# Optimization experiments

Hardware: AMD Instinct MI355X
Metric: run time of the kernel (lower is better)

Reference implementation:

```python
import jax, jax.numpy as jnp
import numpy as np
import math

L, B, E, H = 1024, 16, 512, 8
NUM_REL = 2 * L - 1  # 2047


def setup_inputs() -> dict:
    key = jax.random.key(0)
    ks = jax.random.split(key, 9)
    s = 0.02
    query = jax.random.normal(ks[0], (L, B, E), dtype=jnp.float32)
    return {
        "query": query,
        "key": jax.random.normal(ks[1], (L, B, E), dtype=jnp.float32),
        "value": jax.random.normal(ks[2], (L, B, E), dtype=jnp.float32),
        "in_proj_weight": jax.random.normal(ks[3], (3 * E, E), dtype=jnp.float32) * s,
        "in_proj_bias": jax.random.normal(ks[4], (3 * E,), dtype=jnp.float32) * s,
        "out_proj_weight": jax.random.normal(ks[5], (E, E), dtype=jnp.float32) * s,
        "out_proj_bias": jax.random.normal(ks[6], (E,), dtype=jnp.float32) * s,
        "rpe_weight_table": jax.random.normal(ks[7], (H, NUM_REL), dtype=jnp.float32) * s,
        "rpe_indices": jax.random.randint(ks[8], (L, L), 0, NUM_REL, dtype=jnp.int32),
    }


def _heads(x, w, b):
    # x: (N, Bn, E), w: (E, E), b: (E,) -> (Bn, H, N, d)
    n, bn, e = x.shape
    d = e // H
    y = jnp.einsum('nbe,fe->nbf', x, w) + b
    return y.reshape(n, bn, H, d).transpose(1, 2, 0, 3)


def reference(query, key, value, in_proj_weight, in_proj_bias, out_proj_weight,
              out_proj_bias, rpe_weight_table, rpe_indices):
    l, bn, e = query.shape
    d = e // H
    wq, wk, wv = jnp.split(in_proj_weight, 3, axis=0)
    bq, bk, bv = jnp.split(in_proj_bias, 3, axis=0)
    q = _heads(query, wq, bq)   # (B, H, L, d)
    k = _heads(key, wk, bk)     # (B, H, S, d)
    v = _heads(value, wv, bv)   # (B, H, S, d)
    q = q / math.sqrt(d)
    # rel-pos bias: gather table -> (H, L, S), broadcast over batch
    bias = rpe_weight_table[:, rpe_indices]
    attn = jnp.einsum('bhld,bhsd->bhls', q, k) + bias[None]
    attn = jax.nn.softmax(attn, axis=-1)
    out = jnp.einsum('bhls,bhsd->bhld', attn, v)   # (B, H, L, d)
    out = out.transpose(2, 0, 1, 3).reshape(l, bn, e)  # (L, B, E)
    out = jnp.einsum('lbe,fe->lbf', out, out_proj_weight) + out_proj_bias
    return out
```

## Files before the change

kernel.cpp:

```cpp
#include <hip/hip_runtime.h>
#include <hip/hip_bf16.h>


#define L_SEQ 1024
#define B_N   16
#define E_DIM 512
#define H_N   8
#define NREL  2047

typedef _Float16 f16;
using half8   = __attribute__((ext_vector_type(8))) _Float16;
using floatx4 = __attribute__((ext_vector_type(4))) float;

__device__ __forceinline__ half8 cvt8(const float4 a, const float4 b) {
    half8 h;
    h[0] = (f16)a.x; h[1] = (f16)a.y; h[2] = (f16)a.z; h[3] = (f16)a.w;
    h[4] = (f16)b.x; h[5] = (f16)b.y; h[6] = (f16)b.z; h[7] = (f16)b.w;
    return h;
}

__device__ __forceinline__ void gl_lds16(const void* g, void* l) {
    __builtin_amdgcn_global_load_lds(
        (const __attribute__((address_space(1))) unsigned int*)g,
        (__attribute__((address_space(3))) unsigned int*)l,
        16, 0, 0);
}

__global__ __launch_bounds__(256) void qkv_kernel(
    const float* __restrict__ Xq, const float* __restrict__ Xk, const float* __restrict__ Xv,
    const float* __restrict__ W, const float* __restrict__ Bias,
    f16* __restrict__ Qo, f16* __restrict__ Ko, f16* __restrict__ Vo)
{
    const int flat = blockIdx.x;
    const int xcd  = flat & 7;
    const int slot = flat >> 3;
    const int g    = xcd * 48 + (slot >> 2);
    const int f0   = (slot & 3) << 7;
    const int proj = g >> 7;
    const int n0   = (g & 127) << 7;

    const float* X  = (proj == 0) ? Xq : (proj == 1) ? Xk : Xv;
    const float* Wp = W + (size_t)(proj << 9) * E_DIM;

    __shared__ __align__(16) float As[128 * 32];
    __shared__ __align__(16) float Bs[128 * 32];

    const int tid  = threadIdx.x;
    const int w    = tid >> 6;
    const int lane = tid & 63;
    const int quad = lane >> 4, c = lane & 15;
    const int wm = (w >> 1) << 6, wn = (w & 1) << 6;

    const int lr = lane >> 3;
    const int lc = (lane & 7) ^ lr;
    const float* Xg = X  + (size_t)(n0 + (w << 3) + lr) * E_DIM + (lc << 2);
    const float* Wg = Wp + (size_t)(f0 + (w << 3) + lr) * E_DIM + (lc << 2);

    const int sa0 = (((quad << 1) ^ (c & 7)) << 2);
    const int sa1 = sa0 ^ 4;

    floatx4 acc[4][4] = {};

    for (int k0 = 0; k0 < E_DIM; k0 += 32) {
        __syncthreads();
#pragma unroll
        for (int i = 0; i < 4; ++i) {
            gl_lds16(Xg + (size_t)i * (32 * E_DIM) + k0, &As[((i << 5) + (w << 3)) << 5]);
            gl_lds16(Wg + (size_t)i * (32 * E_DIM) + k0, &Bs[((i << 5) + (w << 3)) << 5]);
        }
        __syncthreads();

        half8 a[4], bfr[4];
#pragma unroll
        for (int mt = 0; mt < 4; ++mt) {
            const int r = (wm + mt * 16 + c) << 5;
            const float4 lo = *reinterpret_cast<const float4*>(&As[r + sa0]);
            const float4 hi = *reinterpret_cast<const float4*>(&As[r + sa1]);
            a[mt] = cvt8(lo, hi);
        }
#pragma unroll
        for (int nt = 0; nt < 4; ++nt) {
            const int r = (wn + nt * 16 + c) << 5;
            const float4 lo = *reinterpret_cast<const float4*>(&Bs[r + sa0]);
            const float4 hi = *reinterpret_cast<const float4*>(&Bs[r + sa1]);
            bfr[nt] = cvt8(lo, hi);
        }
#pragma unroll
        for (int mt = 0; mt < 4; ++mt)
#pragma unroll
            for (int nt = 0; nt < 4; ++nt)
                acc[mt][nt] = __builtin_amdgcn_mfma_f32_16x16x32_f16(a[mt], bfr[nt], acc[mt][nt], 0, 0, 0);
    }

    f16* Dst = (proj == 0) ? Qo : (proj == 1) ? Ko : Vo;
    const float scale = (proj == 0) ? 0.125f : 1.0f;

#pragma unroll
    for (int nt = 0; nt < 4; ++nt) {
        const int fl = f0 + wn + nt * 16 + c;
        const float bj = Bias[(proj << 9) + fl];
        const int h = fl >> 6, d = fl & 63;
#pragma unroll
        for (int mt = 0; mt < 4; ++mt) {
#pragma unroll
            for (int r = 0; r < 4; ++r) {
                const int n = n0 + wm + mt * 16 + quad * 4 + r;
                const int l = n >> 4, b = n & 15;
                Dst[((((size_t)b * H_N + h) * L_SEQ + l) << 6) + d] =
                    (f16)((acc[mt][nt][r] + bj) * scale);
            }
        }
    }
}

__global__ __launch_bounds__(256) void transpose_v(
    const f16* __restrict__ V, f16* __restrict__ Vt)
{
    const int l0 = blockIdx.x << 6;
    const size_t base = (size_t)blockIdx.y << 16;
    __shared__ __align__(16) f16 T[64][72];
    const int tid = threadIdx.x;
    const int r = tid >> 2, co = (tid & 3) << 4;

    const uint4 a0 = *reinterpret_cast<const uint4*>(V + base + (size_t)(l0 + r) * 64 + co);
    const uint4 a1 = *reinterpret_cast<const uint4*>(V + base + (size_t)(l0 + r) * 64 + co + 8);
    *reinterpret_cast<uint4*>(&T[r][co])     = a0;
    *reinterpret_cast<uint4*>(&T[r][co + 8]) = a1;
    __syncthreads();

    union { f16 h[16]; uint4 u[2]; } pk;
#pragma unroll
    for (int j = 0; j < 16; ++j) pk.h[j] = T[co + j][r];
    *reinterpret_cast<uint4*>(Vt + base + (size_t)r * 1024 + l0 + co)     = pk.u[0];
    *reinterpret_cast<uint4*>(Vt + base + (size_t)r * 1024 + l0 + co + 8) = pk.u[1];
}

__global__ __launch_bounds__(256, 3) void attn_kernel(
    const f16* __restrict__ Q, const f16* __restrict__ K, const f16* __restrict__ Vt,
    const int* __restrict__ RPE, const float* __restrict__ Tab, f16* __restrict__ CTX)
{
    const int q0 = blockIdx.x << 7;
    const int bh = blockIdx.y;
    const int b = bh >> 3, h = bh & 7;

    const int tid  = threadIdx.x;
    const int w    = tid >> 6;
    const int lane = tid & 63;
    const int quad = lane >> 4, c = lane & 15;

    __shared__ __align__(16) f16 Ks[64][72];
    __shared__ __align__(16) f16 Vts[64][72];
    __shared__ __align__(16) f16 Pw[4][32][72];
    __shared__ float tab[NREL];

    const size_t base = (size_t)bh << 16;

    for (int i = tid; i < NREL; i += 256) tab[i] = Tab[h * NREL + i];

    const int qg0 = q0 + (w << 5);
    half8 Aq[2][2];
#pragma unroll
    for (int s = 0; s < 2; ++s) {
        const f16* qp = Q + base + (size_t)(qg0 + s * 16 + c) * 64 + quad * 8;
        Aq[s][0] = *reinterpret_cast<const half8*>(qp);
        Aq[s][1] = *reinterpret_cast<const half8*>(qp + 32);
    }

    floatx4 o[2][4] = {};
    float l_part[2][4] = {};

    const int* rp = RPE + (size_t)(qg0 + (quad << 2)) * 1024 + c;

    const int sr = tid >> 2, so = (tid & 3) << 4;
    const f16* kbase = K  + base + (size_t)sr * 64 + so;
    const f16* vbase = Vt + base + (size_t)sr * 1024 + so;

    uint4 pk0 = *reinterpret_cast<const uint4*>(kbase);
    uint4 pk1 = *reinterpret_cast<const uint4*>(kbase + 8);
    uint4 pv0 = *reinterpret_cast<const uint4*>(vbase);
    uint4 pv1 = *reinterpret_cast<const uint4*>(vbase + 8);

    for (int j0 = 0; j0 < L_SEQ; j0 += 64) {
        __syncthreads();
        *reinterpret_cast<uint4*>(&Ks[sr][so])      = pk0;
        *reinterpret_cast<uint4*>(&Ks[sr][so + 8])  = pk1;
        *reinterpret_cast<uint4*>(&Vts[sr][so])     = pv0;
        *reinterpret_cast<uint4*>(&Vts[sr][so + 8]) = pv1;
        __syncthreads();

        if (j0 + 64 < L_SEQ) {
            const f16* kn = kbase + (size_t)(j0 + 64) * 64;
            const f16* vn = vbase + (j0 + 64);
            pk0 = *reinterpret_cast<const uint4*>(kn);
            pk1 = *reinterpret_cast<const uint4*>(kn + 8);
            pv0 = *reinterpret_cast<const uint4*>(vn);
            pv1 = *reinterpret_cast<const uint4*>(vn + 8);
        }

        int idx[2][4][4];
#pragma unroll
        for (int s = 0; s < 2; ++s)
#pragma unroll
            for (int r = 0; r < 4; ++r)
#pragma unroll
                for (int nt = 0; nt < 4; ++nt)
                    idx[s][r][nt] = rp[(size_t)(s * 16 + r) * 1024 + j0 + nt * 16];

        floatx4 sc[2][4];
#pragma unroll
        for (int nt = 0; nt < 4; ++nt) {
            const half8 b0 = *reinterpret_cast<const half8*>(&Ks[nt * 16 + c][quad * 8]);
            const half8 b1 = *reinterpret_cast<const half8*>(&Ks[nt * 16 + c][32 + quad * 8]);
            floatx4 t0 = {}, t1 = {};
            t0 = __builtin_amdgcn_mfma_f32_16x16x32_f16(Aq[0][0], b0, t0, 0, 0, 0);
            t0 = __builtin_amdgcn_mfma_f32_16x16x32_f16(Aq[0][1], b1, t0, 0, 0, 0);
            t1 = __builtin_amdgcn_mfma_f32_16x16x32_f16(Aq[1][0], b0, t1, 0, 0, 0);
            t1 = __builtin_amdgcn_mfma_f32_16x16x32_f16(Aq[1][1], b1, t1, 0, 0, 0);
            sc[0][nt] = t0; sc[1][nt] = t1;
        }

#pragma unroll
        for (int s = 0; s < 2; ++s)
#pragma unroll
            for (int r = 0; r < 4; ++r) {
                float rs = 0.0f;
#pragma unroll
                for (int nt = 0; nt < 4; ++nt) {
                    const float p = __expf(sc[s][nt][r] + tab[idx[s][r][nt]]);
                    rs += p;
                    Pw[w][s * 16 + quad * 4 + r][nt * 16 + c] = (f16)p;
                }
                l_part[s][r] += rs;
            }

        half8 vb[4][2];
#pragma unroll
        for (int nt = 0; nt < 4; ++nt) {
            vb[nt][0] = *reinterpret_cast<const half8*>(&Vts[nt * 16 + c][quad * 8]);
            vb[nt][1] = *reinterpret_cast<const half8*>(&Vts[nt * 16 + c][32 + quad * 8]);
        }
#pragma unroll
        for (int s = 0; s < 2; ++s) {
            const half8 Ap0 = *reinterpret_cast<const half8*>(&Pw[w][s * 16 + c][quad * 8]);
            const half8 Ap1 = *reinterpret_cast<const half8*>(&Pw[w][s * 16 + c][32 + quad * 8]);
#pragma unroll
            for (int nt = 0; nt < 4; ++nt) {
                o[s][nt] = __builtin_amdgcn_mfma_f32_16x16x32_f16(Ap0, vb[nt][0], o[s][nt], 0, 0, 0);
                o[s][nt] = __builtin_amdgcn_mfma_f32_16x16x32_f16(Ap1, vb[nt][1], o[s][nt], 0, 0, 0);
            }
        }
    }

#pragma unroll
    for (int s = 0; s < 2; ++s)
#pragma unroll
        for (int r = 0; r < 4; ++r) {
            float l = l_part[s][r];
            l += __shfl_xor(l, 1); l += __shfl_xor(l, 2);
            l += __shfl_xor(l, 4); l += __shfl_xor(l, 8);
            const float inv = 1.0f / l;
            const int lrow = qg0 + s * 16 + quad * 4 + r;
            f16* dp = CTX + ((size_t)(lrow * 16 + b)) * 512 + h * 64;
#pragma unroll
            for (int nt = 0; nt < 4; ++nt)
                dp[nt * 16 + c] = (f16)(o[s][nt][r] * inv);
        }
}

__global__ __launch_bounds__(256) void out_kernel(
    const f16* __restrict__ X, const float* __restrict__ W, const float* __restrict__ Bias,
    float* __restrict__ Out)
{
    const int flat = blockIdx.x;
    const int xcd  = flat & 7;
    const int slot = flat >> 3;
    const int m    = xcd * 16 + (slot >> 2);
    const int f0   = (slot & 3) << 7;
    const int n0   = m << 7;

    __shared__ __align__(16) f16   As[128 * 32];
    __shared__ __align__(16) float Bs[128 * 32];

    const int tid  = threadIdx.x;
    const int w    = tid >> 6;
    const int lane = tid & 63;
    const int quad = lane >> 4, c = lane & 15;
    const int wm = (w >> 1) << 6, wn = (w & 1) << 6;

    const int ar  = lane >> 2;
    const int ac  = (lane & 3) ^ ((lane >> 3) & 3);
    const f16* Xg = X + (size_t)(n0 + (w << 4) + ar) * E_DIM + (ac << 3);

    const int lr = lane >> 3;
    const int lc = (lane & 7) ^ lr;
    const float* Wg = W + (size_t)(f0 + (w << 3) + lr) * E_DIM + (lc << 2);

    const int sa = ((quad ^ ((c >> 1) & 3)) << 3);
    const int sb0 = (((quad << 1) ^ (c & 7)) << 2);
    const int sb1 = sb0 ^ 4;

    floatx4 acc[4][4] = {};

    for (int k0 = 0; k0 < E_DIM; k0 += 32) {
        __syncthreads();
#pragma unroll
        for (int i = 0; i < 2; ++i)
            gl_lds16(Xg + (size_t)i * (64 * E_DIM) + k0, &As[((i << 6) + (w << 4)) << 5]);
#pragma unroll
        for (int i = 0; i < 4; ++i)
            gl_lds16(Wg + (size_t)i * (32 * E_DIM) + k0, &Bs[((i << 5) + (w << 3)) << 5]);
        __syncthreads();

        half8 a[4], bfr[4];
#pragma unroll
        for (int mt = 0; mt < 4; ++mt) {
            const int r = (wm + mt * 16 + c) << 5;
            a[mt] = *reinterpret_cast<const half8*>(&As[r + sa]);
        }
#pragma unroll
        for (int nt = 0; nt < 4; ++nt) {
            const int r = (wn + nt * 16 + c) << 5;
            const float4 lo = *reinterpret_cast<const float4*>(&Bs[r + sb0]);
            const float4 hi = *reinterpret_cast<const float4*>(&Bs[r + sb1]);
            bfr[nt] = cvt8(lo, hi);
        }
#pragma unroll
        for (int mt = 0; mt < 4; ++mt)
#pragma unroll
            for (int nt = 0; nt < 4; ++nt)
                acc[mt][nt] = __builtin_amdgcn_mfma_f32_16x16x32_f16(a[mt], bfr[nt], acc[mt][nt], 0, 0, 0);
    }

#pragma unroll
    for (int nt = 0; nt < 4; ++nt) {
        const int f = f0 + wn + nt * 16 + c;
        const float bj = Bias[f];
#pragma unroll
        for (int mt = 0; mt < 4; ++mt) {
#pragma unroll
            for (int r = 0; r < 4; ++r) {
                const int n = n0 + wm + mt * 16 + quad * 4 + r;
                Out[(size_t)n * E_DIM + f] = acc[mt][nt][r] + bj;
            }
        }
    }
}

extern "C" void kernel_launch(void* const* d_in, const int* in_sizes, int n_in,
                              void* d_out, int out_size, void* d_ws, size_t ws_size,
                              hipStream_t stream) {
    const float* q_in = (const float*)d_in[0];
    const float* k_in = (const float*)d_in[1];
    const float* v_in = (const float*)d_in[2];
    const float* ipw  = (const float*)d_in[3];
    const float* ipb  = (const float*)d_in[4];
    const float* opw  = (const float*)d_in[5];
    const float* opb  = (const float*)d_in[6];
    const float* tab  = (const float*)d_in[7];
    const int*   rpe  = (const int*)d_in[8];
    float* out = (float*)d_out;

    f16* ws   = (f16*)d_ws;
    f16* Q    = ws;
    f16* K    = ws + 8388608;
    f16* Vt   = ws + 16777216;
    f16* Vtmp = ws + 25165824;
    f16* CTX  = ws + 25165824;

    qkv_kernel<<<dim3(1536), 256, 0, stream>>>(q_in, k_in, v_in, ipw, ipb, Q, K, Vtmp);
    transpose_v<<<dim3(16, 128), 256, 0, stream>>>(Vtmp, Vt);
    attn_kernel<<<dim3(8, 128), 256, 0, stream>>>(Q, K, Vt, rpe, tab, CTX);
    out_kernel<<<dim3(512), 256, 0, stream>>>(CTX, opw, opb, out);
}
```

Measured before the change: 320.4 us.

## Register-prefetch double-buffered fp16 LDS tiles in projection GEMMs; XCD-swizzle attention grid

The QKV and output projection GEMMs stop using direct global-to-LDS fp32 loads with two barriers per step. They now prefetch the next tile into registers, convert to fp16 once before writing into a double-buffered padded LDS tile, and sync with a single lgkmcnt barrier per step, so global loads overlap the MFMA work. The attention launch becomes a flat 1D grid remapped so blocks sharing a batch-head land on the same XCD, which is meant to improve L2 reuse of K and V. The cost is more registers per thread and a different LDS footprint, which could lower occupancy.

Measured after the change: 308.9 us. -3.6%, faster.

```diff
diff --git a/kernel.cpp b/kernel.cpp
--- a/kernel.cpp
+++ b/kernel.cpp
@@ -9,21 +9,21 @@
 #define NREL  2047
 
 typedef _Float16 f16;
+using half4   = __attribute__((ext_vector_type(4))) _Float16;
 using half8   = __attribute__((ext_vector_type(8))) _Float16;
 using floatx4 = __attribute__((ext_vector_type(4))) float;
 
-__device__ __forceinline__ half8 cvt8(const float4 a, const float4 b) {
-    half8 h;
+#define LGKM_BARRIER() do {                                   \
+    asm volatile("s_waitcnt lgkmcnt(0)" ::: "memory");        \
+    __builtin_amdgcn_sched_barrier(0);                        \
+    __builtin_amdgcn_s_barrier();                             \
+    __builtin_amdgcn_sched_barrier(0);                        \
+} while (0)
+
+__device__ __forceinline__ half4 cvt4(const float4 a) {
+    half4 h;
     h[0] = (f16)a.x; h[1] = (f16)a.y; h[2] = (f16)a.z; h[3] = (f16)a.w;
-    h[4] = (f16)b.x; h[5] = (f16)b.y; h[6] = (f16)b.z; h[7] = (f16)b.w;
     return h;
-}
-
-__device__ __forceinline__ void gl_lds16(const void* g, void* l) {
-    __builtin_amdgcn_global_load_lds(
-        (const __attribute__((address_space(1))) unsigned int*)g,
-        (__attribute__((address_space(3))) unsigned int*)l,
-        16, 0, 0);
 }
 
 __global__ __launch_bounds__(256) void qkv_kernel(
@@ -42,8 +42,8 @@
     const float* X  = (proj == 0) ? Xq : (proj == 1) ? Xk : Xv;
     const float* Wp = W + (size_t)(proj << 9) * E_DIM;
 
-    __shared__ __align__(16) float As[128 * 32];
-    __shared__ __align__(16) float Bs[128 * 32];
+    __shared__ __align__(16) f16 As[2][128][40];
+    __shared__ __align__(16) f16 Bs[2][128][40];
 
     const int tid  = threadIdx.x;
     const int w    = tid >> 6;
@@ -51,45 +51,57 @@
     const int quad = lane >> 4, c = lane & 15;
     const int wm = (w >> 1) << 6, wn = (w & 1) << 6;
 
-    const int lr = lane >> 3;
-    const int lc = (lane & 7) ^ lr;
-    const float* Xg = X  + (size_t)(n0 + (w << 3) + lr) * E_DIM + (lc << 2);
-    const float* Wg = Wp + (size_t)(f0 + (w << 3) + lr) * E_DIM + (lc << 2);
-
-    const int sa0 = (((quad << 1) ^ (c & 7)) << 2);
-    const int sa1 = sa0 ^ 4;
+    const int srow = (w << 5) + (lane >> 3);
+    const int scol = (lane & 7) << 2;
+    const float* Xg = X  + (size_t)(n0 + srow) * E_DIM + scol;
+    const float* Wg = Wp + (size_t)(f0 + srow) * E_DIM + scol;
+
+    float4 lx[4], lw[4];
+    auto load_tile = [&](int kk) {
+#pragma unroll
+        for (int i = 0; i < 4; ++i)
+            lx[i] = *reinterpret_cast<const float4*>(Xg + (size_t)(i * 8) * E_DIM + kk);
+#pragma unroll
+        for (int i = 0; i < 4; ++i)
+            lw[i] = *reinterpret_cast<const float4*>(Wg + (size_t)(i * 8) * E_DIM + kk);
+    };
+    auto write_tile = [&](int buf) {
+#pragma unroll
+        for (int i = 0; i < 4; ++i)
+            *reinterpret_cast<half4*>(&As[buf][srow + i * 8][scol]) = cvt4(lx[i]);
+#pragma unroll
+        for (int i = 0; i < 4; ++i)
+            *reinterpret_cast<half4*>(&Bs[buf][srow + i * 8][scol]) = cvt4(lw[i]);
+    };
 
     floatx4 acc[4][4] = {};
 
-    for (int k0 = 0; k0 < E_DIM; k0 += 32) {
-        __syncthreads();
-#pragma unroll
-        for (int i = 0; i < 4; ++i) {
-            gl_lds16(Xg + (size_t)i * (32 * E_DIM) + k0, &As[((i << 5) + (w << 3)) << 5]);
-            gl_lds16(Wg + (size_t)i * (32 * E_DIM) + k0, &Bs[((i << 5) + (w << 3)) << 5]);
-        }
-        __syncthreads();
+    load_tile(0);
+    write_tile(0);
+    load_tile(32);
+    LGKM_BARRIER();
+
+    for (int t = 0; t < 16; ++t) {
+        const int cur = t & 1;
 
         half8 a[4], bfr[4];
 #pragma unroll
-        for (int mt = 0; mt < 4; ++mt) {
-            const int r = (wm + mt * 16 + c) << 5;
-            const float4 lo = *reinterpret_cast<const float4*>(&As[r + sa0]);
-            const float4 hi = *reinterpret_cast<const float4*>(&As[r + sa1]);
-            a[mt] = cvt8(lo, hi);
-        }
-#pragma unroll
-        for (int nt = 0; nt < 4; ++nt) {
-            const int r = (wn + nt * 16 + c) << 5;
-            const float4 lo = *reinterpret_cast<const float4*>(&Bs[r + sa0]);
-            const float4 hi = *reinterpret_cast<const float4*>(&Bs[r + sa1]);
-            bfr[nt] = cvt8(lo, hi);
-        }
+        for (int mt = 0; mt < 4; ++mt)
+            a[mt] = *reinterpret_cast<const half8*>(&As[cur][wm + mt * 16 + c][quad * 8]);
+#pragma unroll
+        for (int nt = 0; nt < 4; ++nt)
+            bfr[nt] = *reinterpret_cast<const half8*>(&Bs[cur][wn + nt * 16 + c][quad * 8]);
 #pragma unroll
         for (int mt = 0; mt < 4; ++mt)
 #pragma unroll
             for (int nt = 0; nt < 4; ++nt)
                 acc[mt][nt] = __builtin_amdgcn_mfma_f32_16x16x32_f16(a[mt], bfr[nt], acc[mt][nt], 0, 0, 0);
+
+        if (t < 15) {
+            write_tile(cur ^ 1);
+            if (t < 14) load_tile((t + 2) * 32);
+        }
+        LGKM_BARRIER();
     }
 
     f16* Dst = (proj == 0) ? Qo : (proj == 1) ? Ko : Vo;
@@ -139,8 +151,11 @@
     const f16* __restrict__ Q, const f16* __restrict__ K, const f16* __restrict__ Vt,
     const int* __restrict__ RPE, const float* __restrict__ Tab, f16* __restrict__ CTX)
 {
-    const int q0 = blockIdx.x << 7;
-    const int bh = blockIdx.y;
+    const int flat = blockIdx.x;
+    const int xcd  = flat & 7;
+    const int slot = flat >> 3;
+    const int q0   = (slot & 7) << 7;
+    const int bh   = ((slot >> 3) << 3) + xcd;
     const int b = bh >> 3, h = bh & 7;
 
     const int tid  = threadIdx.x;
@@ -278,8 +293,8 @@
     const int f0   = (slot & 3) << 7;
     const int n0   = m << 7;
 
-    __shared__ __align__(16) f16   As[128 * 32];
-    __shared__ __align__(16) float Bs[128 * 32];
+    __shared__ __align__(16) f16 As[2][128][40];
+    __shared__ __align__(16) f16 Bs[2][128][40];
 
     const int tid  = threadIdx.x;
     const int w    = tid >> 6;
@@ -287,48 +302,61 @@
     const int quad = lane >> 4, c = lane & 15;
     const int wm = (w >> 1) << 6, wn = (w & 1) << 6;
 
-    const int ar  = lane >> 2;
-    const int ac  = (lane & 3) ^ ((lane >> 3) & 3);
-    const f16* Xg = X + (size_t)(n0 + (w << 4) + ar) * E_DIM + (ac << 3);
-
-    const int lr = lane >> 3;
-    const int lc = (lane & 7) ^ lr;
-    const float* Wg = W + (size_t)(f0 + (w << 3) + lr) * E_DIM + (lc << 2);
-
-    const int sa = ((quad ^ ((c >> 1) & 3)) << 3);
-    const int sb0 = (((quad << 1) ^ (c & 7)) << 2);
-    const int sb1 = sb0 ^ 4;
+    const int arow = (w << 5) + (lane >> 2);
+    const int acol = (lane & 3) << 3;
+    const f16* Xg = X + (size_t)(n0 + arow) * E_DIM + acol;
+
+    const int srow = (w << 5) + (lane >> 3);
+    const int scol = (lane & 7) << 2;
+    const float* Wg = W + (size_t)(f0 + srow) * E_DIM + scol;
+
+    uint4  la[2];
+    float4 lw[4];
+    auto load_tile = [&](int kk) {
+#pragma unroll
+        for (int i = 0; i < 2; ++i)
+            la[i] = *reinterpret_cast<const uint4*>(Xg + (size_t)(i * 16) * E_DIM + kk);
+#pragma unroll
+        for (int i = 0; i < 4; ++i)
+            lw[i] = *reinterpret_cast<const float4*>(Wg + (size_t)(i * 8) * E_DIM + kk);
+    };
+    auto write_tile = [&](int buf) {
+#pragma unroll
+        for (int i = 0; i < 2; ++i)
+            *reinterpret_cast<uint4*>(&As[buf][arow + i * 16][acol]) = la[i];
+#pragma unroll
+        for (int i = 0; i < 4; ++i)
+            *reinterpret_cast<half4*>(&Bs[buf][srow + i * 8][scol]) = cvt4(lw[i]);
+    };
 
     floatx4 acc[4][4] = {};
 
-    for (int k0 = 0; k0 < E_DIM; k0 += 32) {
-        __syncthreads();
-#pragma unroll
-        for (int i = 0; i < 2; ++i)
-            gl_lds16(Xg + (size_t)i * (64 * E_DIM) + k0, &As[((i << 6) + (w << 4)) << 5]);
-#pragma unroll
-        for (int i = 0; i < 4; ++i)
-            gl_lds16(Wg + (size_t)i * (32 * E_DIM) + k0, &Bs[((i << 5) + (w << 3)) << 5]);
-        __syncthreads();
+    load_tile(0);
+    write_tile(0);
+    load_tile(32);
+    LGKM_BARRIER();
+
+    for (int t = 0; t < 16; ++t) {
+        const int cur = t & 1;
 
         half8 a[4], bfr[4];
 #pragma unroll
-        for (int mt = 0; mt < 4; ++mt) {
-            const int r = (wm + mt * 16 + c) << 5;
-            a[mt] = *reinterpret_cast<const half8*>(&As[r + sa]);
-        }
-#pragma unroll
-        for (int nt = 0; nt < 4; ++nt) {
-            const int r = (wn + nt * 16 + c) << 5;
-            const float4 lo = *reinterpret_cast<const float4*>(&Bs[r + sb0]);
-            const float4 hi = *reinterpret_cast<const float4*>(&Bs[r + sb1]);
-            bfr[nt] = cvt8(lo, hi);
-        }
+        for (int mt = 0; mt < 4; ++mt)
+            a[mt] = *reinterpret_cast<const half8*>(&As[cur][wm + mt * 16 + c][quad * 8]);
+#pragma unroll
+        for (int nt = 0; nt < 4; ++nt)
+            bfr[nt] = *reinterpret_cast<const half8*>(&Bs[cur][wn + nt * 16 + c][quad * 8]);
 #pragma unroll
         for (int mt = 0; mt < 4; ++mt)
 #pragma unroll
             for (int nt = 0; nt < 4; ++nt)
                 acc[mt][nt] = __builtin_amdgcn_mfma_f32_16x16x32_f16(a[mt], bfr[nt], acc[mt][nt], 0, 0, 0);
+
+        if (t < 15) {
+            write_tile(cur ^ 1);
+            if (t < 14) load_tile((t + 2) * 32);
+        }
+        LGKM_BARRIER();
     }
 
 #pragma unroll
@@ -369,6 +397,6 @@
 
     qkv_kernel<<<dim3(1536), 256, 0, stream>>>(q_in, k_in, v_in, ipw, ipb, Q, K, Vtmp);
     transpose_v<<<dim3(16, 128), 256, 0, stream>>>(Vtmp, Vt);
-    attn_kernel<<<dim3(8, 128), 256, 0, stream>>>(Q, K, Vt, rpe, tab, CTX);
+    attn_kernel<<<dim3(1024), 256, 0, stream>>>(Q, K, Vt, rpe, tab, CTX);
     out_kernel<<<dim3(512), 256, 0, stream>>>(CTX, opw, opb, out);
 }
```
